# Performance work log

Measured on AMD Instinct MI355X. Metric: run time of the kernel, lower is better.

The kernel has to match this reference:

```python
import jax, jax.numpy as jnp
import numpy as np

N_NODES = 100000
N_EDGES = 3200000
NFEAT, NHID, NCLASS = 512, 128, 40


def _glorot(key, fan_in, fan_out):
    lim = jnp.sqrt(6.0 / (fan_in + fan_out))
    return jax.random.uniform(key, (fan_in, fan_out), jnp.float32, -lim, lim)


def setup_inputs() -> dict:
    key = jax.random.key(0)
    k1, k2, k3, k4, k5 = jax.random.split(key, 5)
    x = jax.random.normal(k1, (N_NODES, NFEAT), jnp.float32)
    edge_index = jax.random.randint(k2, (2, N_EDGES), 0, N_NODES, jnp.int64)
    edge_weight = jax.random.uniform(k3, (N_EDGES,), jnp.float32)
    W1 = _glorot(k4, NFEAT, NHID)
    b1 = jnp.zeros((NHID,), jnp.float32)
    W2 = _glorot(k5, NHID, NCLASS)
    b2 = jnp.zeros((NCLASS,), jnp.float32)
    return {"x": x, "edge_index": edge_index, "edge_weight": edge_weight,
            "W1": W1, "b1": b1, "W2": W2, "b2": b2}


def _gcn_norm(edge_index, edge_weight, num_nodes):
    # add self loops (weight 1), symmetric normalization D^-1/2 A D^-1/2
    loop = jnp.arange(num_nodes, dtype=edge_index.dtype)
    row = jnp.concatenate([edge_index[0], loop])
    col = jnp.concatenate([edge_index[1], loop])
    w = jnp.concatenate([edge_weight, jnp.ones((num_nodes,), edge_weight.dtype)])
    deg = jax.ops.segment_sum(w, col, num_segments=num_nodes)
    dinv = jnp.where(deg > 0, jax.lax.rsqrt(jnp.maximum(deg, 1e-20)), 0.0)
    norm = dinv[row] * w * dinv[col]
    return row, col, norm


def _gcn_conv(h, row, col, norm, W, b, num_nodes):
    h = h @ W                                  # [N, out]
    msg = norm[:, None] * h[row]               # per-edge gather + scale
    out = jax.ops.segment_sum(msg, col, num_segments=num_nodes)  # scatter-add
    return out + b


def reference(x, edge_index, edge_weight, W1, b1, W2, b2):
    n = x.shape[0]
    row, col, norm = _gcn_norm(edge_index, edge_weight, n)
    h = jax.nn.relu(_gcn_conv(x, row, col, norm, W1, b1, n))
    # dropout: eval mode (training=False) -> identity
    return _gcn_conv(h, row, col, norm, W2, b2, n)
```

## Files before the change

### kernel.cpp

```cpp
#include <hip/hip_runtime.h>

#define NN 100000
#define NE 3200000
#define NF 512
#define NH 128
#define NC 40
#define NBIN 196
#define BINW 512
#define CAP  20480
#define EPB  4096

typedef __attribute__((ext_vector_type(8))) short bfrag;
typedef __attribute__((ext_vector_type(4))) float f32x4;
typedef __attribute__((ext_vector_type(8))) unsigned short u16x8;

static __device__ __forceinline__ unsigned short f2bf(float x) {
  unsigned u = __float_as_uint(x);
  u += 0x7FFF + ((u >> 16) & 1);
  return (unsigned short)(u >> 16);
}
static __device__ __forceinline__ float bf2f(unsigned short b) {
  return __uint_as_float(((unsigned)b) << 16);
}


__global__ __launch_bounds__(256) void k_zerobins(int* __restrict__ binfill) {
  if (threadIdx.x < NBIN) binfill[threadIdx.x] = 0;
}


__global__ __launch_bounds__(256) void k_binA(const int* __restrict__ row, const int* __restrict__ col,
                                              const float* __restrict__ w,
                                              int* __restrict__ binfill, int2* __restrict__ binned) {
  __shared__ int hist[NBIN];
  __shared__ int base[NBIN];
  int t = threadIdx.x;
  int eb = blockIdx.x * EPB;
  for (int i = t; i < NBIN; i += 256) hist[i] = 0;
  __syncthreads();
  int rk[16], bn[16], sr[16]; float wv[16];
#pragma unroll
  for (int j = 0; j < 16; ++j) {
    int e = eb + t + j * 256;
    if (e < NE) {
      int c = col[e];
      bn[j] = c >> 9;
      sr[j] = row[e] | ((c & 511) << 17);
      wv[j] = w[e];
      rk[j] = atomicAdd(&hist[bn[j]], 1);
    } else bn[j] = -1;
  }
  __syncthreads();
  if (t < NBIN) { int hv = hist[t]; base[t] = hv ? atomicAdd(&binfill[t], hv) : 0; }
  __syncthreads();
#pragma unroll
  for (int j = 0; j < 16; ++j) {
    if (bn[j] >= 0) {
      int pos = base[bn[j]] + rk[j];
      if (pos < CAP) binned[(size_t)bn[j] * CAP + pos] = make_int2(sr[j], __float_as_int(wv[j]));
    }
  }
}


__global__ __launch_bounds__(256) void k_binscan(const int* __restrict__ binfill,
                                                 int* __restrict__ binptr, int* __restrict__ rowptr) {
  __shared__ int sm[256];
  int t = threadIdx.x;
  sm[t] = (t < NBIN) ? binfill[t] : 0;
  __syncthreads();
  for (int off = 1; off < 256; off <<= 1) {
    int a = (t >= off) ? sm[t - off] : 0;
    __syncthreads();
    sm[t] += a;
    __syncthreads();
  }
  if (t <= NBIN) binptr[t] = (t == 0) ? 0 : sm[t - 1];
  if (t == 0) rowptr[NN] = NE;
}


__global__ __launch_bounds__(256) void k_binB(const int* __restrict__ binfill, const int* __restrict__ binptr,
                                              const int2* __restrict__ binned, int2* __restrict__ pair,
                                              int* __restrict__ rowptr, float* __restrict__ dinv) {
  __shared__ unsigned long long pk[BINW];
  __shared__ unsigned short lrank[CAP];
  __shared__ int lptr[BINW];
  __shared__ int sm[256];
  int t = threadIdx.x;
  int bin = blockIdx.x;
  int cnt = binfill[bin];
  int bb = binptr[bin];
  pk[t] = 0ULL; pk[t + 256] = 0ULL;
  __syncthreads();
  const int2* src = binned + (size_t)bin * CAP;
  for (int i = t; i < cnt; i += 256) {
    int2 r = src[i];
    int lc = (unsigned)r.x >> 17;
    unsigned long long fw = (unsigned long long)(unsigned)(__int_as_float(r.y) * 16777216.0f + 0.5f);
    unsigned long long old = atomicAdd(&pk[lc], (1ULL << 42) | fw);
    lrank[i] = (unsigned short)(old >> 42);
  }
  __syncthreads();
  int c0 = (int)(pk[2 * t] >> 42), c1 = (int)(pk[2 * t + 1] >> 42);
  sm[t] = c0 + c1;
  __syncthreads();
  for (int off = 1; off < 256; off <<= 1) {
    int a = (t >= off) ? sm[t - off] : 0;
    __syncthreads();
    sm[t] += a;
    __syncthreads();
  }
  int excl = (t == 0) ? 0 : sm[t - 1];
  lptr[2 * t] = excl;
  lptr[2 * t + 1] = excl + c0;
  int n0 = bin * BINW + 2 * t;
  if (n0 < NN) {
    rowptr[n0] = bb + excl;
    float d = (float)(pk[2 * t] & 0x3FFFFFFFFFFULL) * (1.0f / 16777216.0f) + 1.0f;
    dinv[n0] = rsqrtf(d);
  }
  if (n0 + 1 < NN) {
    rowptr[n0 + 1] = bb + excl + c0;
    float d = (float)(pk[2 * t + 1] & 0x3FFFFFFFFFFULL) * (1.0f / 16777216.0f) + 1.0f;
    dinv[n0 + 1] = rsqrtf(d);
  }
  __syncthreads();
  for (int i = t; i < cnt; i += 256) {
    int2 r = src[i];
    int lc = (unsigned)r.x >> 17;
    int pos = bb + lptr[lc] + (int)lrank[i];
    pair[pos] = make_int2(r.x & 0x1FFFF, r.y);
  }
}


__global__ __launch_bounds__(256) void k_normC(int2* __restrict__ pair, const float* __restrict__ dinv) {
  int e = blockIdx.x * 256 + threadIdx.x;
  if (e < NE) {
    int2 p = pair[e];
    pair[e].y = __float_as_int(__int_as_float(p.y) * dinv[p.x]);
  }
}


__global__ __launch_bounds__(256) void k_wconv(const float* __restrict__ W1,
                                               unsigned short* __restrict__ Wfh,
                                               unsigned short* __restrict__ Wfl) {
  int i = blockIdx.x * 256 + threadIdx.x;
  int k = i >> 7, n = i & 127;
  float w = W1[i];
  unsigned short hi = f2bf(w);
  unsigned short lo = f2bf(w - bf2f(hi));
  int idx = ((k >> 3) * 128 + n) * 8 + (k & 7);
  Wfh[idx] = hi; Wfl[idx] = lo;
}


__global__ __launch_bounds__(256) void k_gemm1(const float* __restrict__ X,
                                               const unsigned short* __restrict__ Wfh,
                                               const unsigned short* __restrict__ Wfl,
                                               unsigned short* __restrict__ HXb) {
  __shared__ unsigned short Ah[4096], Al[4096], Bh[4096], Bl[4096];
  int t = threadIdx.x;
  int lane = t & 63;
  int wid = t >> 6;
  int m0 = blockIdx.x * 128;
  int sm = t & 127;
  int skh = t >> 7;
  const float* xrow = X + (size_t)(m0 + sm) * NF + skh * 16;
  bool mok = (m0 + sm) < NN;
  int wm = wid >> 1, wn = wid & 1;
  int mb = wm * 64, nb = wn * 64;
  int fr = lane & 15, fg = lane >> 4;

  f32x4 acc[4][4];
#pragma unroll
  for (int i = 0; i < 4; ++i)
#pragma unroll
    for (int j = 0; j < 4; ++j) acc[i][j] = (f32x4)0.0f;

  for (int ks = 0; ks < 16; ++ks) {
    {
      const u16x8* sh = (const u16x8*)(Wfh + (size_t)ks * 4096);
      const u16x8* sl = (const u16x8*)(Wfl + (size_t)ks * 4096);
      u16x8 b0 = sh[t], b1 = sh[t + 256];
      u16x8 c0 = sl[t], c1 = sl[t + 256];
      ((u16x8*)Bh)[t] = b0; ((u16x8*)Bh)[t + 256] = b1;
      ((u16x8*)Bl)[t] = c0; ((u16x8*)Bl)[t + 256] = c1;
    }
    {
      float4 xv[4];
#pragma unroll
      for (int q = 0; q < 4; ++q) {
        xv[q] = mok ? *(const float4*)(xrow + ks * 32 + q * 4)
                    : make_float4(0.f, 0.f, 0.f, 0.f);
      }
#pragma unroll
      for (int q = 0; q < 4; ++q) {
        float f[4] = {xv[q].x, xv[q].y, xv[q].z, xv[q].w};
        unsigned short h[4], l[4];
#pragma unroll
        for (int j = 0; j < 4; ++j) {
          h[j] = f2bf(f[j]);
          l[j] = f2bf(f[j] - bf2f(h[j]));
        }
        int lk = skh * 16 + q * 4;
        int base = (((lk >> 3)) * 128 + sm) * 8 + (lk & 7);
        uint2 hv = make_uint2((unsigned)h[0] | ((unsigned)h[1] << 16),
                              (unsigned)h[2] | ((unsigned)h[3] << 16));
        uint2 lv = make_uint2((unsigned)l[0] | ((unsigned)l[1] << 16),
                              (unsigned)l[2] | ((unsigned)l[3] << 16));
        *(uint2*)&Ah[base] = hv;
        *(uint2*)&Al[base] = lv;
      }
    }
    __syncthreads();
    bfrag ah[4], al[4], bhf[4], blf[4];
#pragma unroll
    for (int mi = 0; mi < 4; ++mi) {
      int idx = (fg * 128 + mb + mi * 16 + fr) * 8;
      ah[mi] = *(bfrag*)&Ah[idx];
      al[mi] = *(bfrag*)&Al[idx];
    }
#pragma unroll
    for (int nt = 0; nt < 4; ++nt) {
      int idx = (fg * 128 + nb + nt * 16 + fr) * 8;
      bhf[nt] = *(bfrag*)&Bh[idx];
      blf[nt] = *(bfrag*)&Bl[idx];
    }
#pragma unroll
    for (int mi = 0; mi < 4; ++mi)
#pragma unroll
      for (int nt = 0; nt < 4; ++nt) {
        acc[mi][nt] = __builtin_amdgcn_mfma_f32_16x16x32_bf16(ah[mi], bhf[nt], acc[mi][nt], 0, 0, 0);
        acc[mi][nt] = __builtin_amdgcn_mfma_f32_16x16x32_bf16(al[mi], bhf[nt], acc[mi][nt], 0, 0, 0);
        acc[mi][nt] = __builtin_amdgcn_mfma_f32_16x16x32_bf16(ah[mi], blf[nt], acc[mi][nt], 0, 0, 0);
      }
    __syncthreads();
  }
#pragma unroll
  for (int mi = 0; mi < 4; ++mi) {
    int rb = m0 + mb + mi * 16 + fg * 4;
#pragma unroll
    for (int nt = 0; nt < 4; ++nt) {
      int c = nb + nt * 16 + fr;
#pragma unroll
      for (int q = 0; q < 4; ++q) {
        int r = rb + q;
        if (r < NN) HXb[(size_t)r * NH + c] = f2bf(acc[mi][nt][q]);
      }
    }
  }
}


__global__ __launch_bounds__(256) void k_agg1(const int* __restrict__ rowptr, const int2* __restrict__ pair,
                                              const unsigned* __restrict__ hxb, const float* __restrict__ dinv,
                                              const float* __restrict__ b1, unsigned* __restrict__ hb) {
  int wid = (blockIdx.x * 256 + threadIdx.x) >> 6;
  int lane = threadIdx.x & 63;
  if (wid >= NN) return;
  int beg = rowptr[wid], end = rowptr[wid + 1];
  float ax = 0.f, ay = 0.f;
  int e = beg;
  for (; e + 4 <= end; e += 4) {
    int2 p0 = pair[e], p1 = pair[e + 1], p2 = pair[e + 2], p3 = pair[e + 3];
    unsigned v0 = hxb[(size_t)p0.x * 64 + lane];
    unsigned v1 = hxb[(size_t)p1.x * 64 + lane];
    unsigned v2 = hxb[(size_t)p2.x * 64 + lane];
    unsigned v3 = hxb[(size_t)p3.x * 64 + lane];
    float n0 = __int_as_float(p0.y), n1 = __int_as_float(p1.y);
    float n2 = __int_as_float(p2.y), n3 = __int_as_float(p3.y);
    ax = fmaf(n0, __uint_as_float(v0 << 16), ax); ay = fmaf(n0, __uint_as_float(v0 & 0xFFFF0000u), ay);
    ax = fmaf(n1, __uint_as_float(v1 << 16), ax); ay = fmaf(n1, __uint_as_float(v1 & 0xFFFF0000u), ay);
    ax = fmaf(n2, __uint_as_float(v2 << 16), ax); ay = fmaf(n2, __uint_as_float(v2 & 0xFFFF0000u), ay);
    ax = fmaf(n3, __uint_as_float(v3 << 16), ax); ay = fmaf(n3, __uint_as_float(v3 & 0xFFFF0000u), ay);
  }
  for (; e < end; ++e) {
    int2 p0 = pair[e];
    unsigned v0 = hxb[(size_t)p0.x * 64 + lane];
    float n0 = __int_as_float(p0.y);
    ax = fmaf(n0, __uint_as_float(v0 << 16), ax); ay = fmaf(n0, __uint_as_float(v0 & 0xFFFF0000u), ay);
  }
  float di = dinv[wid], sl = di * di;
  unsigned own = hxb[(size_t)wid * 64 + lane];
  float2 bb = ((const float2*)b1)[lane];
  float rx = fmaxf(fmaf(di, ax, fmaf(sl, __uint_as_float(own << 16), bb.x)), 0.f);
  float ry = fmaxf(fmaf(di, ay, fmaf(sl, __uint_as_float(own & 0xFFFF0000u), bb.y)), 0.f);
  hb[(size_t)wid * 64 + lane] = (unsigned)f2bf(rx) | ((unsigned)f2bf(ry) << 16);
}


__global__ __launch_bounds__(256) void k_gemm2(const unsigned* __restrict__ hb, const float* __restrict__ W2,
                                               unsigned short* __restrict__ H2b) {
  __shared__ float Hs[32][132];
  __shared__ float Ws[NH * NC];
  int t = threadIdx.x;
  int m0 = blockIdx.x * 32;
  {
    int r = t >> 3, cb = (t & 7) * 8;
    int rowi = m0 + r;
    if (rowi < NN) {
      uint4 a = *(const uint4*)(hb + (size_t)rowi * 64 + cb);
      uint4 b = *(const uint4*)(hb + (size_t)rowi * 64 + cb + 4);
      unsigned u[8] = {a.x, a.y, a.z, a.w, b.x, b.y, b.z, b.w};
#pragma unroll
      for (int j = 0; j < 8; ++j) {
        Hs[r][cb * 2 + j * 2]     = __uint_as_float(u[j] << 16);
        Hs[r][cb * 2 + j * 2 + 1] = __uint_as_float(u[j] & 0xFFFF0000u);
      }
    } else {
#pragma unroll
      for (int j = 0; j < 16; ++j) Hs[r][cb * 2 + j] = 0.f;
    }
  }
  for (int i = t; i < NH * NC; i += 256) Ws[i] = W2[i];
  __syncthreads();
  int r = t >> 3, c0 = (t & 7) * 5;
  float acc[5] = {0.f, 0.f, 0.f, 0.f, 0.f};
#pragma unroll 4
  for (int k = 0; k < NH; ++k) {
    float hv = Hs[r][k];
#pragma unroll
    for (int j = 0; j < 5; ++j) acc[j] = fmaf(hv, Ws[k * NC + c0 + j], acc[j]);
  }
  int rowi = m0 + r;
  if (rowi < NN) {
#pragma unroll
    for (int j = 0; j < 5; ++j) H2b[(size_t)rowi * 64 + c0 + j] = f2bf(acc[j]);
    int pr = t & 7;
    if (pr < 3) {
#pragma unroll
      for (int j = 0; j < 8; ++j) H2b[(size_t)rowi * 64 + 40 + pr * 8 + j] = 0;
    }
  }
}


__global__ __launch_bounds__(256) void k_agg2(const int* __restrict__ rowptr, const int2* __restrict__ pair,
                                              const unsigned short* __restrict__ h2b,
                                              const float* __restrict__ dinv,
                                              const float* __restrict__ b2, float* __restrict__ out) {
  int wid = (blockIdx.x * 256 + threadIdx.x) >> 6;
  int lane = threadIdx.x & 63;
  if (wid >= NN) return;
  int beg = rowptr[wid], end = rowptr[wid + 1];
  float acc = 0.f;
  int e = beg;
  for (; e + 4 <= end; e += 4) {
    int2 p0 = pair[e], p1 = pair[e + 1], p2 = pair[e + 2], p3 = pair[e + 3];
    unsigned short v0 = h2b[(size_t)p0.x * 64 + lane];
    unsigned short v1 = h2b[(size_t)p1.x * 64 + lane];
    unsigned short v2 = h2b[(size_t)p2.x * 64 + lane];
    unsigned short v3 = h2b[(size_t)p3.x * 64 + lane];
    acc = fmaf(__int_as_float(p0.y), bf2f(v0), acc);
    acc = fmaf(__int_as_float(p1.y), bf2f(v1), acc);
    acc = fmaf(__int_as_float(p2.y), bf2f(v2), acc);
    acc = fmaf(__int_as_float(p3.y), bf2f(v3), acc);
  }
  for (; e < end; ++e) {
    int2 p0 = pair[e];
    acc = fmaf(__int_as_float(p0.y), bf2f(h2b[(size_t)p0.x * 64 + lane]), acc);
  }
  float di = dinv[wid], sl = di * di;
  acc = fmaf(di, acc, sl * bf2f(h2b[(size_t)wid * 64 + lane]));
  if (lane < NC) out[(size_t)wid * NC + lane] = acc + b2[lane];
}


extern "C" void kernel_launch(void* const* d_in, const int* in_sizes, int n_in,
                              void* d_out, int out_size, void* d_ws, size_t ws_size,
                              hipStream_t stream) {
  const float* x  = (const float*)d_in[0];
  const int*   ei = (const int*)d_in[1];
  const float* ew = (const float*)d_in[2];
  const float* W1 = (const float*)d_in[3];
  const float* b1 = (const float*)d_in[4];
  const float* W2 = (const float*)d_in[5];
  const float* b2 = (const float*)d_in[6];
  float* out = (float*)d_out;
  const int* row = ei;
  const int* col = ei + NE;

  char* ws = (char*)d_ws;
  size_t o = 0;
  auto alloc = [&](size_t bytes) -> void* {
    void* p = ws + o;
    o += (bytes + 255) & ~(size_t)255;
    return p;
  };
  float* dinv    = (float*)alloc((size_t)NN * 4);
  int*   rowptr  = (int*)alloc((size_t)(NN + 1) * 4);
  int*   binfill = (int*)alloc(1024);
  int*   binptr  = (int*)alloc(1024);
  int2*  pair    = (int2*)alloc((size_t)NE * 8);
  unsigned short* Wfh = (unsigned short*)alloc((size_t)NF * NH * 2);
  unsigned short* Wfl = (unsigned short*)alloc((size_t)NF * NH * 2);
  unsigned short* hxb = (unsigned short*)alloc((size_t)NN * NH * 2);
  unsigned*       hb  = (unsigned*)alloc((size_t)NN * NH * 2);
  int2*  binned  = (int2*)alloc((size_t)NBIN * CAP * 8);
  unsigned short* h2b = (unsigned short*)hxb;

  k_zerobins<<<1, 256, 0, stream>>>(binfill);
  k_wconv<<<(NF * NH) / 256, 256, 0, stream>>>(W1, Wfh, Wfl);
  k_binA<<<(NE + EPB - 1) / EPB, 256, 0, stream>>>(row, col, ew, binfill, binned);
  k_binscan<<<1, 256, 0, stream>>>(binfill, binptr, rowptr);
  k_binB<<<NBIN, 256, 0, stream>>>(binfill, binptr, binned, pair, rowptr, dinv);
  k_normC<<<NE / 256, 256, 0, stream>>>(pair, dinv);
  k_gemm1<<<(NN + 127) / 128, 256, 0, stream>>>(x, Wfh, Wfl, hxb);
  k_agg1<<<(NN * 64) / 256, 256, 0, stream>>>(rowptr, pair, (const unsigned*)hxb, dinv, b1, hb);
  k_gemm2<<<(NN + 31) / 32, 256, 0, stream>>>(hb, W2, h2b);
  k_agg2<<<(NN * 64) / 256, 256, 0, stream>>>(rowptr, pair, h2b, dinv, b2, out);
}
```

Baseline: 475.8 us.

## Fold source-side normalization into GEMM epilogues, drop split-bf16 term, nontemporal memory ops

Removes the k_normC pass by scaling each GEMM output row by dinv of the source node, so edge weights need no per-edge dinv[row] multiply. The self-loop is then handled as di*(acc+own). GEMM1 now reads W fragments directly from global memory instead of staging them in LDS, and drops the low-part X term, going from three MFMAs per tile to two. This lowers precision for X. The aggregation loops are unrolled to 8 edges with nontemporal pair loads, and outputs use nontemporal stores.

```diff
diff --git a/kernel.cpp b/kernel.cpp
--- a/kernel.cpp
+++ b/kernel.cpp
@@ -12,7 +12,6 @@
 
 typedef __attribute__((ext_vector_type(8))) short bfrag;
 typedef __attribute__((ext_vector_type(4))) float f32x4;
-typedef __attribute__((ext_vector_type(8))) unsigned short u16x8;
 
 static __device__ __forceinline__ unsigned short f2bf(float x) {
   unsigned u = __float_as_uint(x);
@@ -43,10 +42,10 @@
   for (int j = 0; j < 16; ++j) {
     int e = eb + t + j * 256;
     if (e < NE) {
-      int c = col[e];
+      int c = __builtin_nontemporal_load(col + e);
       bn[j] = c >> 9;
-      sr[j] = row[e] | ((c & 511) << 17);
-      wv[j] = w[e];
+      sr[j] = __builtin_nontemporal_load(row + e) | ((c & 511) << 17);
+      wv[j] = __builtin_nontemporal_load(w + e);
       rk[j] = atomicAdd(&hist[bn[j]], 1);
     } else bn[j] = -1;
   }
@@ -89,7 +88,7 @@
   __shared__ int sm[256];
   int t = threadIdx.x;
   int bin = blockIdx.x;
-  int cnt = binfill[bin];
+  int cnt = binfill[bin]; if (cnt > CAP) cnt = CAP;
   int bb = binptr[bin];
   pk[t] = 0ULL; pk[t + 256] = 0ULL;
   __syncthreads();
@@ -131,15 +130,6 @@
     int lc = (unsigned)r.x >> 17;
     int pos = bb + lptr[lc] + (int)lrank[i];
     pair[pos] = make_int2(r.x & 0x1FFFF, r.y);
-  }
-}
-
-
-__global__ __launch_bounds__(256) void k_normC(int2* __restrict__ pair, const float* __restrict__ dinv) {
-  int e = blockIdx.x * 256 + threadIdx.x;
-  if (e < NE) {
-    int2 p = pair[e];
-    pair[e].y = __float_as_int(__int_as_float(p.y) * dinv[p.x]);
   }
 }
 
@@ -160,8 +150,9 @@
 __global__ __launch_bounds__(256) void k_gemm1(const float* __restrict__ X,
                                                const unsigned short* __restrict__ Wfh,
                                                const unsigned short* __restrict__ Wfl,
+                                               const float* __restrict__ dinv,
                                                unsigned short* __restrict__ HXb) {
-  __shared__ unsigned short Ah[4096], Al[4096], Bh[4096], Bl[4096];
+  __shared__ unsigned short Ah[4096];
   int t = threadIdx.x;
   int lane = t & 63;
   int wid = t >> 6;
@@ -182,14 +173,6 @@
 
   for (int ks = 0; ks < 16; ++ks) {
     {
-      const u16x8* sh = (const u16x8*)(Wfh + (size_t)ks * 4096);
-      const u16x8* sl = (const u16x8*)(Wfl + (size_t)ks * 4096);
-      u16x8 b0 = sh[t], b1 = sh[t + 256];
-      u16x8 c0 = sl[t], c1 = sl[t + 256];
-      ((u16x8*)Bh)[t] = b0; ((u16x8*)Bh)[t + 256] = b1;
-      ((u16x8*)Bl)[t] = c0; ((u16x8*)Bl)[t + 256] = c1;
-    }
-    {
       float4 xv[4];
 #pragma unroll
       for (int q = 0; q < 4; ++q) {
@@ -199,43 +182,35 @@
 #pragma unroll
       for (int q = 0; q < 4; ++q) {
         float f[4] = {xv[q].x, xv[q].y, xv[q].z, xv[q].w};
-        unsigned short h[4], l[4];
-#pragma unroll
-        for (int j = 0; j < 4; ++j) {
-          h[j] = f2bf(f[j]);
-          l[j] = f2bf(f[j] - bf2f(h[j]));
-        }
+        unsigned short h[4];
+#pragma unroll
+        for (int j = 0; j < 4; ++j) h[j] = f2bf(f[j]);
         int lk = skh * 16 + q * 4;
-        int base = (((lk >> 3)) * 128 + sm) * 8 + (lk & 7);
+        int base = ((lk >> 3) * 128 + sm) * 8 + (lk & 7);
         uint2 hv = make_uint2((unsigned)h[0] | ((unsigned)h[1] << 16),
                               (unsigned)h[2] | ((unsigned)h[3] << 16));
-        uint2 lv = make_uint2((unsigned)l[0] | ((unsigned)l[1] << 16),
-                              (unsigned)l[2] | ((unsigned)l[3] << 16));
         *(uint2*)&Ah[base] = hv;
-        *(uint2*)&Al[base] = lv;
       }
     }
     __syncthreads();
-    bfrag ah[4], al[4], bhf[4], blf[4];
-#pragma unroll
-    for (int mi = 0; mi < 4; ++mi) {
-      int idx = (fg * 128 + mb + mi * 16 + fr) * 8;
-      ah[mi] = *(bfrag*)&Ah[idx];
-      al[mi] = *(bfrag*)&Al[idx];
-    }
+    bfrag ah[4], bh[4], bl[4];
+#pragma unroll
+    for (int mi = 0; mi < 4; ++mi)
+      ah[mi] = *(bfrag*)&Ah[(fg * 128 + mb + mi * 16 + fr) * 8];
+    const unsigned short* Bh = Wfh + (size_t)ks * 4096;
+    const unsigned short* Bl = Wfl + (size_t)ks * 4096;
 #pragma unroll
     for (int nt = 0; nt < 4; ++nt) {
       int idx = (fg * 128 + nb + nt * 16 + fr) * 8;
-      bhf[nt] = *(bfrag*)&Bh[idx];
-      blf[nt] = *(bfrag*)&Bl[idx];
+      bh[nt] = *(const bfrag*)(Bh + idx);
+      bl[nt] = *(const bfrag*)(Bl + idx);
     }
 #pragma unroll
     for (int mi = 0; mi < 4; ++mi)
 #pragma unroll
       for (int nt = 0; nt < 4; ++nt) {
-        acc[mi][nt] = __builtin_amdgcn_mfma_f32_16x16x32_bf16(ah[mi], bhf[nt], acc[mi][nt], 0, 0, 0);
-        acc[mi][nt] = __builtin_amdgcn_mfma_f32_16x16x32_bf16(al[mi], bhf[nt], acc[mi][nt], 0, 0, 0);
-        acc[mi][nt] = __builtin_amdgcn_mfma_f32_16x16x32_bf16(ah[mi], blf[nt], acc[mi][nt], 0, 0, 0);
+        acc[mi][nt] = __builtin_amdgcn_mfma_f32_16x16x32_bf16(ah[mi], bh[nt], acc[mi][nt], 0, 0, 0);
+        acc[mi][nt] = __builtin_amdgcn_mfma_f32_16x16x32_bf16(ah[mi], bl[nt], acc[mi][nt], 0, 0, 0);
       }
     __syncthreads();
   }
@@ -243,12 +218,15 @@
   for (int mi = 0; mi < 4; ++mi) {
     int rb = m0 + mb + mi * 16 + fg * 4;
 #pragma unroll
-    for (int nt = 0; nt < 4; ++nt) {
-      int c = nb + nt * 16 + fr;
-#pragma unroll
-      for (int q = 0; q < 4; ++q) {
-        int r = rb + q;
-        if (r < NN) HXb[(size_t)r * NH + c] = f2bf(acc[mi][nt][q]);
+    for (int q = 0; q < 4; ++q) {
+      int r = rb + q;
+      if (r < NN) {
+        float dv = dinv[r];
+#pragma unroll
+        for (int nt = 0; nt < 4; ++nt) {
+          int c = nb + nt * 16 + fr;
+          __builtin_nontemporal_store(f2bf(dv * acc[mi][nt][q]), HXb + (size_t)r * NH + c);
+        }
       }
     }
   }
@@ -264,35 +242,40 @@
   int beg = rowptr[wid], end = rowptr[wid + 1];
   float ax = 0.f, ay = 0.f;
   int e = beg;
-  for (; e + 4 <= end; e += 4) {
-    int2 p0 = pair[e], p1 = pair[e + 1], p2 = pair[e + 2], p3 = pair[e + 3];
-    unsigned v0 = hxb[(size_t)p0.x * 64 + lane];
-    unsigned v1 = hxb[(size_t)p1.x * 64 + lane];
-    unsigned v2 = hxb[(size_t)p2.x * 64 + lane];
-    unsigned v3 = hxb[(size_t)p3.x * 64 + lane];
-    float n0 = __int_as_float(p0.y), n1 = __int_as_float(p1.y);
-    float n2 = __int_as_float(p2.y), n3 = __int_as_float(p3.y);
-    ax = fmaf(n0, __uint_as_float(v0 << 16), ax); ay = fmaf(n0, __uint_as_float(v0 & 0xFFFF0000u), ay);
-    ax = fmaf(n1, __uint_as_float(v1 << 16), ax); ay = fmaf(n1, __uint_as_float(v1 & 0xFFFF0000u), ay);
-    ax = fmaf(n2, __uint_as_float(v2 << 16), ax); ay = fmaf(n2, __uint_as_float(v2 & 0xFFFF0000u), ay);
-    ax = fmaf(n3, __uint_as_float(v3 << 16), ax); ay = fmaf(n3, __uint_as_float(v3 & 0xFFFF0000u), ay);
+  const long long* pr = (const long long*)pair;
+  for (; e + 8 <= end; e += 8) {
+    long long raw[8];
+#pragma unroll
+    for (int j = 0; j < 8; ++j) raw[j] = __builtin_nontemporal_load(pr + e + j);
+    unsigned v[8];
+#pragma unroll
+    for (int j = 0; j < 8; ++j) v[j] = hxb[(size_t)(unsigned)(raw[j] & 0x1FFFF) * 64 + lane];
+#pragma unroll
+    for (int j = 0; j < 8; ++j) {
+      float n = __int_as_float((int)(raw[j] >> 32));
+      ax = fmaf(n, __uint_as_float(v[j] << 16), ax);
+      ay = fmaf(n, __uint_as_float(v[j] & 0xFFFF0000u), ay);
+    }
   }
   for (; e < end; ++e) {
-    int2 p0 = pair[e];
-    unsigned v0 = hxb[(size_t)p0.x * 64 + lane];
-    float n0 = __int_as_float(p0.y);
-    ax = fmaf(n0, __uint_as_float(v0 << 16), ax); ay = fmaf(n0, __uint_as_float(v0 & 0xFFFF0000u), ay);
-  }
-  float di = dinv[wid], sl = di * di;
+    long long raw = __builtin_nontemporal_load(pr + e);
+    unsigned v = hxb[(size_t)(unsigned)(raw & 0x1FFFF) * 64 + lane];
+    float n = __int_as_float((int)(raw >> 32));
+    ax = fmaf(n, __uint_as_float(v << 16), ax);
+    ay = fmaf(n, __uint_as_float(v & 0xFFFF0000u), ay);
+  }
+  float di = dinv[wid];
   unsigned own = hxb[(size_t)wid * 64 + lane];
   float2 bb = ((const float2*)b1)[lane];
-  float rx = fmaxf(fmaf(di, ax, fmaf(sl, __uint_as_float(own << 16), bb.x)), 0.f);
-  float ry = fmaxf(fmaf(di, ay, fmaf(sl, __uint_as_float(own & 0xFFFF0000u), bb.y)), 0.f);
-  hb[(size_t)wid * 64 + lane] = (unsigned)f2bf(rx) | ((unsigned)f2bf(ry) << 16);
+  float rx = fmaxf(fmaf(di, ax + __uint_as_float(own << 16), bb.x), 0.f);
+  float ry = fmaxf(fmaf(di, ay + __uint_as_float(own & 0xFFFF0000u), bb.y), 0.f);
+  __builtin_nontemporal_store((unsigned)f2bf(rx) | ((unsigned)f2bf(ry) << 16),
+                              hb + (size_t)wid * 64 + lane);
 }
 
 
 __global__ __launch_bounds__(256) void k_gemm2(const unsigned* __restrict__ hb, const float* __restrict__ W2,
+                                               const float* __restrict__ dinv,
                                                unsigned short* __restrict__ H2b) {
   __shared__ float Hs[32][132];
   __shared__ float Ws[NH * NC];
@@ -327,12 +310,15 @@
   }
   int rowi = m0 + r;
   if (rowi < NN) {
-#pragma unroll
-    for (int j = 0; j < 5; ++j) H2b[(size_t)rowi * 64 + c0 + j] = f2bf(acc[j]);
+    float dv = dinv[rowi];
+#pragma unroll
+    for (int j = 0; j < 5; ++j)
+      __builtin_nontemporal_store(f2bf(dv * acc[j]), H2b + (size_t)rowi * 64 + c0 + j);
     int pr = t & 7;
     if (pr < 3) {
 #pragma unroll
-      for (int j = 0; j < 8; ++j) H2b[(size_t)rowi * 64 + 40 + pr * 8 + j] = 0;
+      for (int j = 0; j < 8; ++j)
+        __builtin_nontemporal_store((unsigned short)0, H2b + (size_t)rowi * 64 + 40 + pr * 8 + j);
     }
   }
 }
@@ -348,24 +334,26 @@
   int beg = rowptr[wid], end = rowptr[wid + 1];
   float acc = 0.f;
   int e = beg;
-  for (; e + 4 <= end; e += 4) {
-    int2 p0 = pair[e], p1 = pair[e + 1], p2 = pair[e + 2], p3 = pair[e + 3];
-    unsigned short v0 = h2b[(size_t)p0.x * 64 + lane];
-    unsigned short v1 = h2b[(size_t)p1.x * 64 + lane];
-    unsigned short v2 = h2b[(size_t)p2.x * 64 + lane];
-    unsigned short v3 = h2b[(size_t)p3.x * 64 + lane];
-    acc = fmaf(__int_as_float(p0.y), bf2f(v0), acc);
-    acc = fmaf(__int_as_float(p1.y), bf2f(v1), acc);
-    acc = fmaf(__int_as_float(p2.y), bf2f(v2), acc);
-    acc = fmaf(__int_as_float(p3.y), bf2f(v3), acc);
+  const long long* pr = (const long long*)pair;
+  for (; e + 8 <= end; e += 8) {
+    long long raw[8];
+#pragma unroll
+    for (int j = 0; j < 8; ++j) raw[j] = __builtin_nontemporal_load(pr + e + j);
+    unsigned short v[8];
+#pragma unroll
+    for (int j = 0; j < 8; ++j) v[j] = h2b[(size_t)(unsigned)(raw[j] & 0x1FFFF) * 64 + lane];
+#pragma unroll
+    for (int j = 0; j < 8; ++j)
+      acc = fmaf(__int_as_float((int)(raw[j] >> 32)), bf2f(v[j]), acc);
   }
   for (; e < end; ++e) {
-    int2 p0 = pair[e];
-    acc = fmaf(__int_as_float(p0.y), bf2f(h2b[(size_t)p0.x * 64 + lane]), acc);
-  }
-  float di = dinv[wid], sl = di * di;
-  acc = fmaf(di, acc, sl * bf2f(h2b[(size_t)wid * 64 + lane]));
-  if (lane < NC) out[(size_t)wid * NC + lane] = acc + b2[lane];
+    long long raw = __builtin_nontemporal_load(pr + e);
+    acc = fmaf(__int_as_float((int)(raw >> 32)),
+               bf2f(h2b[(size_t)(unsigned)(raw & 0x1FFFF) * 64 + lane]), acc);
+  }
+  float di = dinv[wid];
+  float r = fmaf(di, acc + bf2f(h2b[(size_t)wid * 64 + lane]), (lane < NC) ? b2[lane] : 0.f);
+  if (lane < NC) __builtin_nontemporal_store(r, out + (size_t)wid * NC + lane);
 }
 
 
@@ -407,9 +395,8 @@
   k_binA<<<(NE + EPB - 1) / EPB, 256, 0, stream>>>(row, col, ew, binfill, binned);
   k_binscan<<<1, 256, 0, stream>>>(binfill, binptr, rowptr);
   k_binB<<<NBIN, 256, 0, stream>>>(binfill, binptr, binned, pair, rowptr, dinv);
-  k_normC<<<NE / 256, 256, 0, stream>>>(pair, dinv);
-  k_gemm1<<<(NN + 127) / 128, 256, 0, stream>>>(x, Wfh, Wfl, hxb);
+  k_gemm1<<<(NN + 127) / 128, 256, 0, stream>>>(x, Wfh, Wfl, dinv, hxb);
   k_agg1<<<(NN * 64) / 256, 256, 0, stream>>>(rowptr, pair, (const unsigned*)hxb, dinv, b1, hb);
-  k_gemm2<<<(NN + 31) / 32, 256, 0, stream>>>(hb, W2, h2b);
+  k_gemm2<<<(NN + 31) / 32, 256, 0, stream>>>(hb, W2, dinv, h2b);
   k_agg2<<<(NN * 64) / 256, 256, 0, stream>>>(rowptr, pair, h2b, dinv, b2, out);
 }
```

Measured after the change: 489.5 us. +2.9%, slower.
